# Kernel tuning notes

Hardware: AMD Instinct MI355X
Metric: run time of the kernel (lower is better)

## Reference

```python
import jax, jax.numpy as jnp
import numpy as np

N_NODES = 100000
N_EDGES = 600000
IN_CH = 128
HID = 64
NEG_SLOPE = 0.01  # nn.LeakyReLU default


def setup_inputs() -> dict:
    key = jax.random.key(0)
    k1, k2, k3, k4, k5, k6, k7, k8 = jax.random.split(key, 8)
    s1 = 1.0 / np.sqrt(IN_CH)
    s2 = 1.0 / np.sqrt(HID)
    return {
        "z": jax.random.normal(k1, (N_NODES, IN_CH), dtype=jnp.float32),
        "edge_index": jax.random.randint(k2, (2, N_EDGES), 0, N_NODES, dtype=jnp.int64),
        "W1l": jax.random.uniform(k3, (HID, IN_CH), jnp.float32, -s1, s1),
        "b1l": jax.random.uniform(k4, (HID,), jnp.float32, -s1, s1),
        "W1r": jax.random.uniform(k5, (HID, IN_CH), jnp.float32, -s1, s1),
        "b1r": jax.random.uniform(k6, (HID,), jnp.float32, -s1, s1),
        "W2": jax.random.uniform(k7, (1, HID), jnp.float32, -s2, s2),
        "b2": jax.random.uniform(k8, (1,), jnp.float32, -s2, s2),
    }


def reference(z, edge_index, W1l, b1l, W1r, b1r, W2, b2):
    # gather src/dst node features: [E, in_ch]
    zl = z[edge_index[0]]
    zr = z[edge_index[1]]
    # dual linear + add: [E, hid]
    h = jnp.einsum('ei,hi->eh', zl, W1l) + b1l + jnp.einsum('ei,hi->eh', zr, W1r) + b1r
    h = jnp.where(h >= 0, h, NEG_SLOPE * h)  # LeakyReLU
    out = jnp.einsum('eh,oh->eo', h, W2) + b2  # [E, 1]
    return jax.nn.sigmoid(out)
```

## Files before the change

### kernel.cpp

```cpp
#include <hip/hip_runtime.h>
#include <math.h>

#define N_NODES 100000
#define N_EDGES 600000
#define IN_CH 128
#define HID 64
#define NEG_SLOPE 0.01f

typedef float4 f4;
typedef unsigned short u16;
typedef unsigned int u32;
typedef __attribute__((ext_vector_type(8))) short bf16x8;
typedef __attribute__((ext_vector_type(4))) float f32x4;

__device__ __forceinline__ float lrelu(float x) {
    return fmaxf(x, NEG_SLOPE * x);
}
__device__ __forceinline__ float uasf(u32 w) { return __uint_as_float(w); }

__device__ __forceinline__ u32 cvt_pk(float lo, float hi) {
    u32 r;
    asm("v_cvt_pk_bf16_f32 %0, %1, %2" : "=v"(r) : "v"(lo), "v"(hi));
    return r;
}
__device__ __forceinline__ u16 f2bf(float f) {
    u32 x = __float_as_uint(f);
    return (u16)((x + 0x7fffu + ((x >> 16) & 1u)) >> 16);
}

__device__ __forceinline__ int load_idx(const void* ei, int is64, int pos) {
    if (is64) return (int)((const long long*)ei)[pos];
    return ((const int*)ei)[pos];
}

__global__ __launch_bounds__(256) void node_proj_kernel(
    const float* __restrict__ z, const float* __restrict__ W1l,
    const float* __restrict__ b1l, const float* __restrict__ W1r,
    const float* __restrict__ b1r, const u32* __restrict__ ei_words,
    int* __restrict__ flag, u16* __restrict__ pcomb) {
    __shared__ uint4 wt[128 * 16];
    __shared__ uint4 zt[64 * 16];
    __shared__ u32 red;

    const int tid = threadIdx.x;

    if (blockIdx.x == 0) {
        if (tid == 0) red = 0u;
        __syncthreads();
        u32 acc = 0u;
        #pragma unroll
        for (int i = 0; i < 8; ++i)
            acc |= ei_words[(i * 256 + tid) * 2 + 1];
        atomicOr(&red, acc);
        __syncthreads();
        if (tid == 0) *flag = (red == 0u) ? 1 : 0;
    }

    #pragma unroll
    for (int i = 0; i < 8; ++i) {
        int gidx = tid + i * 256;
        int row = gidx >> 4, gr = gidx & 15;
        const float* wsrc = (row < 64) ? (W1l + row * IN_CH)
                                       : (W1r + (row - 64) * IN_CH);
        f4 a = ((const f4*)wsrc)[gr * 2];
        f4 b = ((const f4*)wsrc)[gr * 2 + 1];
        uint4 p;
        p.x = cvt_pk(a.x, a.y); p.y = cvt_pk(a.z, a.w);
        p.z = cvt_pk(b.x, b.y); p.w = cvt_pk(b.z, b.w);
        wt[(row << 4) | (gr ^ (row & 15))] = p;
    }

    const int base = blockIdx.x * 64;
    #pragma unroll
    for (int i = 0; i < 4; ++i) {
        int gidx = tid + i * 256;
        int row = gidx >> 4, gr = gidx & 15;
        int node = base + row;
        if (node >= N_NODES) node = N_NODES - 1;
        f4 a = ((const f4*)z)[node * 32 + gr * 2];
        f4 b = ((const f4*)z)[node * 32 + gr * 2 + 1];
        uint4 p;
        p.x = cvt_pk(a.x, a.y); p.y = cvt_pk(a.z, a.w);
        p.z = cvt_pk(b.x, b.y); p.w = cvt_pk(b.z, b.w);
        zt[(row << 4) | (gr ^ (row & 15))] = p;
    }
    __syncthreads();

    const int wave = tid >> 6, lane = tid & 63;
    const int m = lane & 15, g = lane >> 4;

    f32x4 acc[4][2];
    #pragma unroll
    for (int n4 = 0; n4 < 4; ++n4)
        #pragma unroll
        for (int c2 = 0; c2 < 2; ++c2) acc[n4][c2] = {0.f, 0.f, 0.f, 0.f};

    #pragma unroll
    for (int kk = 0; kk < 4; ++kk) {
        const int gran = (kk << 2) | g;
        bf16x8 zf[4], wf[2];
        #pragma unroll
        for (int n4 = 0; n4 < 4; ++n4)
            zf[n4] = *(const bf16x8*)&zt[((((n4 << 4) | m)) << 4) | (gran ^ m)];
        #pragma unroll
        for (int c2 = 0; c2 < 2; ++c2) {
            int R = (wave << 5) + (c2 << 4) + m;
            wf[c2] = *(const bf16x8*)&wt[(R << 4) | (gran ^ m)];
        }
        #pragma unroll
        for (int n4 = 0; n4 < 4; ++n4)
            #pragma unroll
            for (int c2 = 0; c2 < 2; ++c2)
                acc[n4][c2] = __builtin_amdgcn_mfma_f32_16x16x32_bf16(
                    wf[c2], zf[n4], acc[n4][c2], 0, 0, 0);
    }

    const int colbase = wave << 5;
    #pragma unroll
    for (int c2 = 0; c2 < 2; ++c2) {
        const int col0 = colbase + (c2 << 4) + (g << 2);
        const float* bsrc = (colbase < 64) ? (b1l + col0) : (b1r + col0 - 64);
        f4 bb = *(const f4*)bsrc;
        #pragma unroll
        for (int n4 = 0; n4 < 4; ++n4) {
            int node = base + (n4 << 4) + m;
            if (node < N_NODES) {
                uint2 v;
                v.x = cvt_pk(acc[n4][c2][0] + bb.x, acc[n4][c2][1] + bb.y);
                v.y = cvt_pk(acc[n4][c2][2] + bb.z, acc[n4][c2][3] + bb.w);
                *(uint2*)(pcomb + (size_t)node * 128 + col0) = v;
            }
        }
    }
}

__device__ __forceinline__ float edot(uint4 a, uint4 b, f4 w0, f4 w1) {
    float s;
    s  = lrelu(uasf(a.x << 16) + uasf(b.x << 16)) * w0.x;
    s += lrelu(uasf(a.x & 0xffff0000u) + uasf(b.x & 0xffff0000u)) * w0.y;
    s += lrelu(uasf(a.y << 16) + uasf(b.y << 16)) * w0.z;
    s += lrelu(uasf(a.y & 0xffff0000u) + uasf(b.y & 0xffff0000u)) * w0.w;
    s += lrelu(uasf(a.z << 16) + uasf(b.z << 16)) * w1.x;
    s += lrelu(uasf(a.z & 0xffff0000u) + uasf(b.z & 0xffff0000u)) * w1.y;
    s += lrelu(uasf(a.w << 16) + uasf(b.w << 16)) * w1.z;
    s += lrelu(uasf(a.w & 0xffff0000u) + uasf(b.w & 0xffff0000u)) * w1.w;
    return s;
}

__global__ __launch_bounds__(256) void edge_kernel(
    const void* __restrict__ ei, const int* __restrict__ flag,
    const u16* __restrict__ pcomb, const float* __restrict__ W2,
    const float* __restrict__ b2, float* __restrict__ out) {
    int t = blockIdx.x * 256 + threadIdx.x;
    int pair = t >> 3;
    int c = t & 7;
    if (pair >= N_EDGES / 2) return;
    const int is64 = *flag;
    int s0, s1, d0, d1;
    if (is64) {
        const longlong2* p = (const longlong2*)ei;
        longlong2 sp = p[pair];
        longlong2 dp = p[N_EDGES / 2 + pair];
        s0 = (int)sp.x; s1 = (int)sp.y; d0 = (int)dp.x; d1 = (int)dp.y;
    } else {
        const int2* p = (const int2*)ei;
        int2 sp = p[pair];
        int2 dp = p[N_EDGES / 2 + pair];
        s0 = sp.x; s1 = sp.y; d0 = dp.x; d1 = dp.y;
    }
    const uint4* pc4 = (const uint4*)pcomb;
    uint4 a0 = pc4[s0 * 16 + c];
    uint4 b0 = pc4[d0 * 16 + 8 + c];
    uint4 a1 = pc4[s1 * 16 + c];
    uint4 b1 = pc4[d1 * 16 + 8 + c];
    f4 w0 = ((const f4*)W2)[c * 2];
    f4 w1 = ((const f4*)W2)[c * 2 + 1];
    float r0 = edot(a0, b0, w0, w1);
    float r1 = edot(a1, b1, w0, w1);
    r0 += __shfl_xor(r0, 4, 8);
    r0 += __shfl_xor(r0, 2, 8);
    r0 += __shfl_xor(r0, 1, 8);
    r1 += __shfl_xor(r1, 4, 8);
    r1 += __shfl_xor(r1, 2, 8);
    r1 += __shfl_xor(r1, 1, 8);
    if (c == 0) {
        float bb = b2[0];
        float2 o;
        o.x = 1.f / (1.f + __expf(-(r0 + bb)));
        o.y = 1.f / (1.f + __expf(-(r1 + bb)));
        *(float2*)(out + pair * 2) = o;
    }
}

__global__ void detect_idx_kernel(const u32* __restrict__ ei_words,
                                  int* __restrict__ flag) {
    __shared__ u32 red;
    if (threadIdx.x == 0) red = 0u;
    __syncthreads();
    u32 acc = 0u;
    #pragma unroll
    for (int i = 0; i < 8; ++i)
        acc |= ei_words[(i * 256 + threadIdx.x) * 2 + 1];
    atomicOr(&red, acc);
    __syncthreads();
    if (threadIdx.x == 0) *flag = (red == 0u) ? 1 : 0;
}

__global__ __launch_bounds__(256) void edge_fallback_kernel(
    const float* __restrict__ z, const void* __restrict__ ei,
    const int* __restrict__ flag, const float* __restrict__ W1l,
    const float* __restrict__ b1l, const float* __restrict__ W1r,
    const float* __restrict__ b1r, const float* __restrict__ W2,
    const float* __restrict__ b2, float* __restrict__ out) {
    __shared__ f4 Wl4[64 * 32];
    __shared__ f4 Wr4[64 * 32];
    const int tid = threadIdx.x;
    #pragma unroll
    for (int i = 0; i < 8; ++i) {
        int gg = tid + i * 256;
        int h = gg >> 5, v = gg & 31;
        int slot = (h << 5) | (v ^ (h & 7));
        Wl4[slot] = ((const f4*)W1l)[gg];
        Wr4[slot] = ((const f4*)W1r)[gg];
    }
    __syncthreads();
    const int wave = tid >> 6, lane = tid & 63;
    int e = blockIdx.x * 4 + wave;
    if (e >= N_EDGES) return;
    const int is64 = (flag != nullptr) ? *flag : 0;
    int src = load_idx(ei, is64, e);
    int dst = load_idx(ei, is64, N_EDGES + e);
    float accl = 0.f, accr = 0.f;
    #pragma unroll 4
    for (int v = 0; v < 32; ++v) {
        f4 wl = Wl4[(lane << 5) | (v ^ (lane & 7))];
        f4 wr = Wr4[(lane << 5) | (v ^ (lane & 7))];
        f4 zl = ((const f4*)z)[src * 32 + v];
        f4 zr = ((const f4*)z)[dst * 32 + v];
        accl += wl.x * zl.x + wl.y * zl.y + wl.z * zl.z + wl.w * zl.w;
        accr += wr.x * zr.x + wr.y * zr.y + wr.z * zr.z + wr.w * zr.w;
    }
    float h = lrelu(accl + b1l[lane] + accr + b1r[lane]) * W2[lane];
    #pragma unroll
    for (int off = 32; off; off >>= 1) h += __shfl_xor(h, off, 64);
    if (lane == 0) out[e] = 1.f / (1.f + __expf(-(h + b2[0])));
}

extern "C" void kernel_launch(void* const* d_in, const int* in_sizes, int n_in,
                              void* d_out, int out_size, void* d_ws,
                              size_t ws_size, hipStream_t stream) {
    const float* z   = (const float*)d_in[0];
    const void*  ei  = d_in[1];
    const float* W1l = (const float*)d_in[2];
    const float* b1l = (const float*)d_in[3];
    const float* W1r = (const float*)d_in[4];
    const float* b1r = (const float*)d_in[5];
    const float* W2  = (const float*)d_in[6];
    const float* b2  = (const float*)d_in[7];
    float* out = (float*)d_out;

    const size_t pcomb_bytes = (size_t)N_NODES * 128 * sizeof(u16);
    const size_t need = pcomb_bytes + 256;

    if (ws_size >= need) {
        u16* pcomb = (u16*)d_ws;
        int* flag = (int*)((char*)d_ws + pcomb_bytes);
        node_proj_kernel<<<(N_NODES + 63) / 64, 256, 0, stream>>>(
            z, W1l, b1l, W1r, b1r, (const u32*)ei, flag, pcomb);
        edge_kernel<<<(N_EDGES / 2 * 8 + 255) / 256, 256, 0, stream>>>(
            ei, flag, pcomb, W2, b2, out);
    } else if (ws_size >= 256) {
        int* flag = (int*)d_ws;
        detect_idx_kernel<<<1, 256, 0, stream>>>((const u32*)ei, flag);
        edge_fallback_kernel<<<(N_EDGES + 3) / 4, 256, 0, stream>>>(
            z, ei, flag, W1l, b1l, W1r, b1r, W2, b2, out);
    } else {
        edge_fallback_kernel<<<(N_EDGES + 3) / 4, 256, 0, stream>>>(
            z, ei, nullptr, W1l, b1l, W1r, b1r, W2, b2, out);
    }
}
```

Measured before the change: 45.67 us.

## Fuse node projection and edge scoring into one persistent cooperative kernel

Replaces the two-kernel path with a single cooperative persistent kernel. It loops over node tiles to compute the bf16 projections, waits at a grid-wide sync, then scores edges with a grid-stride loop handling four edges per 8-lane group. Each block detects the index width itself, so the weights are converted to bf16 in LDS once per block rather than once per tile, and one kernel launch is saved. The costs are a grid barrier, host-side occupancy queries on every call, and fewer resident blocks than the old launch for latency hiding. The fallback edge kernel also now processes four edges per group.

```diff
diff --git a/kernel.cpp b/kernel.cpp
--- a/kernel.cpp
+++ b/kernel.cpp
@@ -1,4 +1,5 @@
 #include <hip/hip_runtime.h>
+#include <hip/hip_cooperative_groups.h>
 #include <math.h>
 
 #define N_NODES 100000
@@ -23,37 +24,45 @@
     asm("v_cvt_pk_bf16_f32 %0, %1, %2" : "=v"(r) : "v"(lo), "v"(hi));
     return r;
 }
-__device__ __forceinline__ u16 f2bf(float f) {
-    u32 x = __float_as_uint(f);
-    return (u16)((x + 0x7fffu + ((x >> 16) & 1u)) >> 16);
-}
 
 __device__ __forceinline__ int load_idx(const void* ei, int is64, int pos) {
     if (is64) return (int)((const long long*)ei)[pos];
     return ((const int*)ei)[pos];
 }
 
-__global__ __launch_bounds__(256) void node_proj_kernel(
+__device__ __forceinline__ float edot(uint4 a, uint4 b, f4 w0, f4 w1) {
+    float s;
+    s  = lrelu(uasf(a.x << 16) + uasf(b.x << 16)) * w0.x;
+    s += lrelu(uasf(a.x & 0xffff0000u) + uasf(b.x & 0xffff0000u)) * w0.y;
+    s += lrelu(uasf(a.y << 16) + uasf(b.y << 16)) * w0.z;
+    s += lrelu(uasf(a.y & 0xffff0000u) + uasf(b.y & 0xffff0000u)) * w0.w;
+    s += lrelu(uasf(a.z << 16) + uasf(b.z << 16)) * w1.x;
+    s += lrelu(uasf(a.z & 0xffff0000u) + uasf(b.z & 0xffff0000u)) * w1.y;
+    s += lrelu(uasf(a.w << 16) + uasf(b.w << 16)) * w1.z;
+    s += lrelu(uasf(a.w & 0xffff0000u) + uasf(b.w & 0xffff0000u)) * w1.w;
+    return s;
+}
+
+__global__ __launch_bounds__(256) void fused_kernel(
     const float* __restrict__ z, const float* __restrict__ W1l,
     const float* __restrict__ b1l, const float* __restrict__ W1r,
-    const float* __restrict__ b1r, const u32* __restrict__ ei_words,
-    int* __restrict__ flag, u16* __restrict__ pcomb) {
+    const float* __restrict__ b1r, const void* __restrict__ ei,
+    const float* __restrict__ W2, const float* __restrict__ b2,
+    float* __restrict__ out, u16* __restrict__ pcomb) {
     __shared__ uint4 wt[128 * 16];
     __shared__ uint4 zt[64 * 16];
-    __shared__ u32 red;
+    __shared__ u32 sflag;
 
     const int tid = threadIdx.x;
 
-    if (blockIdx.x == 0) {
-        if (tid == 0) red = 0u;
-        __syncthreads();
+    if (tid == 0) sflag = 0u;
+    __syncthreads();
+    {
         u32 acc = 0u;
-        #pragma unroll
-        for (int i = 0; i < 8; ++i)
-            acc |= ei_words[(i * 256 + tid) * 2 + 1];
-        atomicOr(&red, acc);
-        __syncthreads();
-        if (tid == 0) *flag = (red == 0u) ? 1 : 0;
+        const u32* w = (const u32*)ei;
+        #pragma unroll
+        for (int i = 0; i < 8; ++i) acc |= w[(i * 256 + tid) * 2 + 1];
+        if (acc) atomicOr(&sflag, 1u);
     }
 
     #pragma unroll
@@ -70,6 +79,162 @@
         wt[(row << 4) | (gr ^ (row & 15))] = p;
     }
 
+    const int wave = tid >> 6, lane = tid & 63;
+    const int m = lane & 15, g = lane >> 4;
+
+    for (int tile = blockIdx.x; tile * 64 < N_NODES; tile += gridDim.x) {
+        const int base = tile * 64;
+        #pragma unroll
+        for (int i = 0; i < 4; ++i) {
+            int gidx = tid + i * 256;
+            int row = gidx >> 4, gr = gidx & 15;
+            int node = base + row;
+            if (node >= N_NODES) node = N_NODES - 1;
+            f4 a = ((const f4*)z)[node * 32 + gr * 2];
+            f4 b = ((const f4*)z)[node * 32 + gr * 2 + 1];
+            uint4 p;
+            p.x = cvt_pk(a.x, a.y); p.y = cvt_pk(a.z, a.w);
+            p.z = cvt_pk(b.x, b.y); p.w = cvt_pk(b.z, b.w);
+            zt[(row << 4) | (gr ^ (row & 15))] = p;
+        }
+        __syncthreads();
+
+        f32x4 acc[4][2];
+        #pragma unroll
+        for (int n4 = 0; n4 < 4; ++n4)
+            #pragma unroll
+            for (int c2 = 0; c2 < 2; ++c2) acc[n4][c2] = {0.f, 0.f, 0.f, 0.f};
+
+        #pragma unroll
+        for (int kk = 0; kk < 4; ++kk) {
+            const int gran = (kk << 2) | g;
+            bf16x8 zf[4], wf[2];
+            #pragma unroll
+            for (int n4 = 0; n4 < 4; ++n4)
+                zf[n4] = *(const bf16x8*)&zt[(((n4 << 4) | m) << 4) | (gran ^ m)];
+            #pragma unroll
+            for (int c2 = 0; c2 < 2; ++c2) {
+                int R = (wave << 5) + (c2 << 4) + m;
+                wf[c2] = *(const bf16x8*)&wt[(R << 4) | (gran ^ m)];
+            }
+            #pragma unroll
+            for (int n4 = 0; n4 < 4; ++n4)
+                #pragma unroll
+                for (int c2 = 0; c2 < 2; ++c2)
+                    acc[n4][c2] = __builtin_amdgcn_mfma_f32_16x16x32_bf16(
+                        wf[c2], zf[n4], acc[n4][c2], 0, 0, 0);
+        }
+
+        const int colbase = wave << 5;
+        #pragma unroll
+        for (int c2 = 0; c2 < 2; ++c2) {
+            const int col0 = colbase + (c2 << 4) + (g << 2);
+            const float* bsrc = (colbase < 64) ? (b1l + col0) : (b1r + col0 - 64);
+            f4 bb = *(const f4*)bsrc;
+            #pragma unroll
+            for (int n4 = 0; n4 < 4; ++n4) {
+                int node = base + (n4 << 4) + m;
+                if (node < N_NODES) {
+                    uint2 v;
+                    v.x = cvt_pk(acc[n4][c2][0] + bb.x, acc[n4][c2][1] + bb.y);
+                    v.y = cvt_pk(acc[n4][c2][2] + bb.z, acc[n4][c2][3] + bb.w);
+                    *(uint2*)(pcomb + (size_t)node * 128 + col0) = v;
+                }
+            }
+        }
+        __syncthreads();
+    }
+
+    const int is64 = (sflag == 0u);
+
+    cooperative_groups::this_grid().sync();
+
+    const int c = tid & 7;
+    const f4 w0 = ((const f4*)W2)[c * 2];
+    const f4 w1 = ((const f4*)W2)[c * 2 + 1];
+    const float bb = b2[0];
+    const int nthreads = gridDim.x * 256;
+    const int qstride = nthreads >> 3;
+    const int NQ = N_EDGES / 4;
+
+    for (int q = (blockIdx.x * 256 + tid) >> 3; q < NQ; q += qstride) {
+        int s[4], d[4];
+        if (is64) {
+            const longlong2* p = (const longlong2*)ei;
+            longlong2 p0 = p[2 * q], p1 = p[2 * q + 1];
+            longlong2 q0 = p[N_EDGES / 2 + 2 * q], q1 = p[N_EDGES / 2 + 2 * q + 1];
+            s[0] = (int)p0.x; s[1] = (int)p0.y; s[2] = (int)p1.x; s[3] = (int)p1.y;
+            d[0] = (int)q0.x; d[1] = (int)q0.y; d[2] = (int)q1.x; d[3] = (int)q1.y;
+        } else {
+            int4 sp = ((const int4*)ei)[q];
+            int4 dp = ((const int4*)ei)[N_EDGES / 4 + q];
+            s[0] = sp.x; s[1] = sp.y; s[2] = sp.z; s[3] = sp.w;
+            d[0] = dp.x; d[1] = dp.y; d[2] = dp.z; d[3] = dp.w;
+        }
+        const uint4* pc4 = (const uint4*)pcomb;
+        uint4 a0 = pc4[s[0] * 16 + c],     a1 = pc4[s[1] * 16 + c];
+        uint4 a2 = pc4[s[2] * 16 + c],     a3 = pc4[s[3] * 16 + c];
+        uint4 e0 = pc4[d[0] * 16 + 8 + c], e1 = pc4[d[1] * 16 + 8 + c];
+        uint4 e2 = pc4[d[2] * 16 + 8 + c], e3 = pc4[d[3] * 16 + 8 + c];
+        float r0 = edot(a0, e0, w0, w1);
+        float r1 = edot(a1, e1, w0, w1);
+        float r2 = edot(a2, e2, w0, w1);
+        float r3 = edot(a3, e3, w0, w1);
+        #pragma unroll
+        for (int off = 4; off; off >>= 1) {
+            r0 += __shfl_xor(r0, off, 8);
+            r1 += __shfl_xor(r1, off, 8);
+            r2 += __shfl_xor(r2, off, 8);
+            r3 += __shfl_xor(r3, off, 8);
+        }
+        if (c == 0) {
+            f4 o;
+            o.x = 1.f / (1.f + __expf(-(r0 + bb)));
+            o.y = 1.f / (1.f + __expf(-(r1 + bb)));
+            o.z = 1.f / (1.f + __expf(-(r2 + bb)));
+            o.w = 1.f / (1.f + __expf(-(r3 + bb)));
+            *(f4*)(out + q * 4) = o;
+        }
+    }
+}
+
+__global__ __launch_bounds__(256) void node_proj_kernel(
+    const float* __restrict__ z, const float* __restrict__ W1l,
+    const float* __restrict__ b1l, const float* __restrict__ W1r,
+    const float* __restrict__ b1r, const u32* __restrict__ ei_words,
+    int* __restrict__ flag, u16* __restrict__ pcomb) {
+    __shared__ uint4 wt[128 * 16];
+    __shared__ uint4 zt[64 * 16];
+    __shared__ u32 red;
+
+    const int tid = threadIdx.x;
+
+    if (blockIdx.x == 0) {
+        if (tid == 0) red = 0u;
+        __syncthreads();
+        u32 acc = 0u;
+        #pragma unroll
+        for (int i = 0; i < 8; ++i)
+            acc |= ei_words[(i * 256 + tid) * 2 + 1];
+        atomicOr(&red, acc);
+        __syncthreads();
+        if (tid == 0) *flag = (red == 0u) ? 1 : 0;
+    }
+
+    #pragma unroll
+    for (int i = 0; i < 8; ++i) {
+        int gidx = tid + i * 256;
+        int row = gidx >> 4, gr = gidx & 15;
+        const float* wsrc = (row < 64) ? (W1l + row * IN_CH)
+                                       : (W1r + (row - 64) * IN_CH);
+        f4 a = ((const f4*)wsrc)[gr * 2];
+        f4 b = ((const f4*)wsrc)[gr * 2 + 1];
+        uint4 p;
+        p.x = cvt_pk(a.x, a.y); p.y = cvt_pk(a.z, a.w);
+        p.z = cvt_pk(b.x, b.y); p.w = cvt_pk(b.z, b.w);
+        wt[(row << 4) | (gr ^ (row & 15))] = p;
+    }
+
     const int base = blockIdx.x * 64;
     #pragma unroll
     for (int i = 0; i < 4; ++i) {
@@ -101,7 +266,7 @@
         bf16x8 zf[4], wf[2];
         #pragma unroll
         for (int n4 = 0; n4 < 4; ++n4)
-            zf[n4] = *(const bf16x8*)&zt[((((n4 << 4) | m)) << 4) | (gran ^ m)];
+            zf[n4] = *(const bf16x8*)&zt[(((n4 << 4) | m) << 4) | (gran ^ m)];
         #pragma unroll
         for (int c2 = 0; c2 < 2; ++c2) {
             int R = (wave << 5) + (c2 << 4) + m;
@@ -134,61 +299,54 @@
     }
 }
 
-__device__ __forceinline__ float edot(uint4 a, uint4 b, f4 w0, f4 w1) {
-    float s;
-    s  = lrelu(uasf(a.x << 16) + uasf(b.x << 16)) * w0.x;
-    s += lrelu(uasf(a.x & 0xffff0000u) + uasf(b.x & 0xffff0000u)) * w0.y;
-    s += lrelu(uasf(a.y << 16) + uasf(b.y << 16)) * w0.z;
-    s += lrelu(uasf(a.y & 0xffff0000u) + uasf(b.y & 0xffff0000u)) * w0.w;
-    s += lrelu(uasf(a.z << 16) + uasf(b.z << 16)) * w1.x;
-    s += lrelu(uasf(a.z & 0xffff0000u) + uasf(b.z & 0xffff0000u)) * w1.y;
-    s += lrelu(uasf(a.w << 16) + uasf(b.w << 16)) * w1.z;
-    s += lrelu(uasf(a.w & 0xffff0000u) + uasf(b.w & 0xffff0000u)) * w1.w;
-    return s;
-}
-
-__global__ __launch_bounds__(256) void edge_kernel(
+__global__ __launch_bounds__(256) void edge_quad_kernel(
     const void* __restrict__ ei, const int* __restrict__ flag,
     const u16* __restrict__ pcomb, const float* __restrict__ W2,
     const float* __restrict__ b2, float* __restrict__ out) {
     int t = blockIdx.x * 256 + threadIdx.x;
-    int pair = t >> 3;
+    int q = t >> 3;
     int c = t & 7;
-    if (pair >= N_EDGES / 2) return;
+    if (q >= N_EDGES / 4) return;
     const int is64 = *flag;
-    int s0, s1, d0, d1;
+    int s[4], d[4];
     if (is64) {
         const longlong2* p = (const longlong2*)ei;
-        longlong2 sp = p[pair];
-        longlong2 dp = p[N_EDGES / 2 + pair];
-        s0 = (int)sp.x; s1 = (int)sp.y; d0 = (int)dp.x; d1 = (int)dp.y;
+        longlong2 p0 = p[2 * q], p1 = p[2 * q + 1];
+        longlong2 q0 = p[N_EDGES / 2 + 2 * q], q1 = p[N_EDGES / 2 + 2 * q + 1];
+        s[0] = (int)p0.x; s[1] = (int)p0.y; s[2] = (int)p1.x; s[3] = (int)p1.y;
+        d[0] = (int)q0.x; d[1] = (int)q0.y; d[2] = (int)q1.x; d[3] = (int)q1.y;
     } else {
-        const int2* p = (const int2*)ei;
-        int2 sp = p[pair];
-        int2 dp = p[N_EDGES / 2 + pair];
-        s0 = sp.x; s1 = sp.y; d0 = dp.x; d1 = dp.y;
+        int4 sp = ((const int4*)ei)[q];
+        int4 dp = ((const int4*)ei)[N_EDGES / 4 + q];
+        s[0] = sp.x; s[1] = sp.y; s[2] = sp.z; s[3] = sp.w;
+        d[0] = dp.x; d[1] = dp.y; d[2] = dp.z; d[3] = dp.w;
     }
     const uint4* pc4 = (const uint4*)pcomb;
-    uint4 a0 = pc4[s0 * 16 + c];
-    uint4 b0 = pc4[d0 * 16 + 8 + c];
-    uint4 a1 = pc4[s1 * 16 + c];
-    uint4 b1 = pc4[d1 * 16 + 8 + c];
+    uint4 a0 = pc4[s[0] * 16 + c],     a1 = pc4[s[1] * 16 + c];
+    uint4 a2 = pc4[s[2] * 16 + c],     a3 = pc4[s[3] * 16 + c];
+    uint4 e0 = pc4[d[0] * 16 + 8 + c], e1 = pc4[d[1] * 16 + 8 + c];
+    uint4 e2 = pc4[d[2] * 16 + 8 + c], e3 = pc4[d[3] * 16 + 8 + c];
     f4 w0 = ((const f4*)W2)[c * 2];
     f4 w1 = ((const f4*)W2)[c * 2 + 1];
-    float r0 = edot(a0, b0, w0, w1);
-    float r1 = edot(a1, b1, w0, w1);
-    r0 += __shfl_xor(r0, 4, 8);
-    r0 += __shfl_xor(r0, 2, 8);
-    r0 += __shfl_xor(r0, 1, 8);
-    r1 += __shfl_xor(r1, 4, 8);
-    r1 += __shfl_xor(r1, 2, 8);
-    r1 += __shfl_xor(r1, 1, 8);
+    float r0 = edot(a0, e0, w0, w1);
+    float r1 = edot(a1, e1, w0, w1);
+    float r2 = edot(a2, e2, w0, w1);
+    float r3 = edot(a3, e3, w0, w1);
+    #pragma unroll
+    for (int off = 4; off; off >>= 1) {
+        r0 += __shfl_xor(r0, off, 8);
+        r1 += __shfl_xor(r1, off, 8);
+        r2 += __shfl_xor(r2, off, 8);
+        r3 += __shfl_xor(r3, off, 8);
+    }
     if (c == 0) {
         float bb = b2[0];
-        float2 o;
+        f4 o;
         o.x = 1.f / (1.f + __expf(-(r0 + bb)));
         o.y = 1.f / (1.f + __expf(-(r1 + bb)));
-        *(float2*)(out + pair * 2) = o;
+        o.z = 1.f / (1.f + __expf(-(r2 + bb)));
+        o.w = 1.f / (1.f + __expf(-(r3 + bb)));
+        *(f4*)(out + q * 4) = o;
     }
 }
 
@@ -265,10 +423,27 @@
     if (ws_size >= need) {
         u16* pcomb = (u16*)d_ws;
         int* flag = (int*)((char*)d_ws + pcomb_bytes);
-        node_proj_kernel<<<(N_NODES + 63) / 64, 256, 0, stream>>>(
-            z, W1l, b1l, W1r, b1r, (const u32*)ei, flag, pcomb);
-        edge_kernel<<<(N_EDGES / 2 * 8 + 255) / 256, 256, 0, stream>>>(
-            ei, flag, pcomb, W2, b2, out);
+
+        int maxB = 0, nCU = 0, dev = 0;
+        hipGetDevice(&dev);
+        hipDeviceGetAttribute(&nCU, hipDeviceAttributeMultiprocessorCount, dev);
+        hipOccupancyMaxActiveBlocksPerMultiprocessor(&maxB, fused_kernel, 256, 0);
+        int grid = (maxB > 0 && nCU > 0) ? maxB * nCU : 0;
+
+        hipError_t e = hipErrorUnknown;
+        if (grid >= 64) {
+            void* args[] = {(void*)&z,  (void*)&W1l, (void*)&b1l, (void*)&W1r,
+                            (void*)&b1r, (void*)&ei, (void*)&W2,  (void*)&b2,
+                            (void*)&out, (void*)&pcomb};
+            e = hipLaunchCooperativeKernel((const void*)fused_kernel, dim3(grid),
+                                           dim3(256), args, 0, stream);
+        }
+        if (e != hipSuccess) {
+            node_proj_kernel<<<(N_NODES + 63) / 64, 256, 0, stream>>>(
+                z, W1l, b1l, W1r, b1r, (const u32*)ei, flag, pcomb);
+            edge_quad_kernel<<<(N_EDGES / 4 * 8 + 255) / 256, 256, 0, stream>>>(
+                ei, flag, pcomb, W2, b2, out);
+        }
     } else if (ws_size >= 256) {
         int* flag = (int*)d_ws;
         detect_idx_kernel<<<1, 256, 0, stream>>>((const u32*)ei, flag);
```

New measurement: 105.3 us. +130.6%, slower.

## Persistent node projection with register-resident weights; process four edges per thread group

Applied to the files above, without the earlier changes.

The node projection becomes a persistent grid of 1024 blocks that converts W1l/W1r to bf16 once into registers and then loops over node tiles. Before, every one of ~1563 blocks reloaded and converted the full weight matrix through LDS. The edge kernel now handles four edges per 8-lane group instead of two, using wider index loads and float4 output stores to get more memory-level parallelism. The cost is more registers per thread, which can lower occupancy, and fewer blocks in the edge kernel.

```diff
diff --git a/kernel.cpp b/kernel.cpp
--- a/kernel.cpp
+++ b/kernel.cpp
@@ -6,6 +6,7 @@
 #define IN_CH 128
 #define HID 64
 #define NEG_SLOPE 0.01f
+#define NP_GRID 1024
 
 typedef float4 f4;
 typedef unsigned short u16;
@@ -23,115 +24,10 @@
     asm("v_cvt_pk_bf16_f32 %0, %1, %2" : "=v"(r) : "v"(lo), "v"(hi));
     return r;
 }
-__device__ __forceinline__ u16 f2bf(float f) {
-    u32 x = __float_as_uint(f);
-    return (u16)((x + 0x7fffu + ((x >> 16) & 1u)) >> 16);
-}
 
 __device__ __forceinline__ int load_idx(const void* ei, int is64, int pos) {
     if (is64) return (int)((const long long*)ei)[pos];
     return ((const int*)ei)[pos];
-}
-
-__global__ __launch_bounds__(256) void node_proj_kernel(
-    const float* __restrict__ z, const float* __restrict__ W1l,
-    const float* __restrict__ b1l, const float* __restrict__ W1r,
-    const float* __restrict__ b1r, const u32* __restrict__ ei_words,
-    int* __restrict__ flag, u16* __restrict__ pcomb) {
-    __shared__ uint4 wt[128 * 16];
-    __shared__ uint4 zt[64 * 16];
-    __shared__ u32 red;
-
-    const int tid = threadIdx.x;
-
-    if (blockIdx.x == 0) {
-        if (tid == 0) red = 0u;
-        __syncthreads();
-        u32 acc = 0u;
-        #pragma unroll
-        for (int i = 0; i < 8; ++i)
-            acc |= ei_words[(i * 256 + tid) * 2 + 1];
-        atomicOr(&red, acc);
-        __syncthreads();
-        if (tid == 0) *flag = (red == 0u) ? 1 : 0;
-    }
-
-    #pragma unroll
-    for (int i = 0; i < 8; ++i) {
-        int gidx = tid + i * 256;
-        int row = gidx >> 4, gr = gidx & 15;
-        const float* wsrc = (row < 64) ? (W1l + row * IN_CH)
-                                       : (W1r + (row - 64) * IN_CH);
-        f4 a = ((const f4*)wsrc)[gr * 2];
-        f4 b = ((const f4*)wsrc)[gr * 2 + 1];
-        uint4 p;
-        p.x = cvt_pk(a.x, a.y); p.y = cvt_pk(a.z, a.w);
-        p.z = cvt_pk(b.x, b.y); p.w = cvt_pk(b.z, b.w);
-        wt[(row << 4) | (gr ^ (row & 15))] = p;
-    }
-
-    const int base = blockIdx.x * 64;
-    #pragma unroll
-    for (int i = 0; i < 4; ++i) {
-        int gidx = tid + i * 256;
-        int row = gidx >> 4, gr = gidx & 15;
-        int node = base + row;
-        if (node >= N_NODES) node = N_NODES - 1;
-        f4 a = ((const f4*)z)[node * 32 + gr * 2];
-        f4 b = ((const f4*)z)[node * 32 + gr * 2 + 1];
-        uint4 p;
-        p.x = cvt_pk(a.x, a.y); p.y = cvt_pk(a.z, a.w);
-        p.z = cvt_pk(b.x, b.y); p.w = cvt_pk(b.z, b.w);
-        zt[(row << 4) | (gr ^ (row & 15))] = p;
-    }
-    __syncthreads();
-
-    const int wave = tid >> 6, lane = tid & 63;
-    const int m = lane & 15, g = lane >> 4;
-
-    f32x4 acc[4][2];
-    #pragma unroll
-    for (int n4 = 0; n4 < 4; ++n4)
-        #pragma unroll
-        for (int c2 = 0; c2 < 2; ++c2) acc[n4][c2] = {0.f, 0.f, 0.f, 0.f};
-
-    #pragma unroll
-    for (int kk = 0; kk < 4; ++kk) {
-        const int gran = (kk << 2) | g;
-        bf16x8 zf[4], wf[2];
-        #pragma unroll
-        for (int n4 = 0; n4 < 4; ++n4)
-            zf[n4] = *(const bf16x8*)&zt[((((n4 << 4) | m)) << 4) | (gran ^ m)];
-        #pragma unroll
-        for (int c2 = 0; c2 < 2; ++c2) {
-            int R = (wave << 5) + (c2 << 4) + m;
-            wf[c2] = *(const bf16x8*)&wt[(R << 4) | (gran ^ m)];
-        }
-        #pragma unroll
-        for (int n4 = 0; n4 < 4; ++n4)
-            #pragma unroll
-            for (int c2 = 0; c2 < 2; ++c2)
-                acc[n4][c2] = __builtin_amdgcn_mfma_f32_16x16x32_bf16(
-                    wf[c2], zf[n4], acc[n4][c2], 0, 0, 0);
-    }
-
-    const int colbase = wave << 5;
-    #pragma unroll
-    for (int c2 = 0; c2 < 2; ++c2) {
-        const int col0 = colbase + (c2 << 4) + (g << 2);
-        const float* bsrc = (colbase < 64) ? (b1l + col0) : (b1r + col0 - 64);
-        f4 bb = *(const f4*)bsrc;
-        #pragma unroll
-        for (int n4 = 0; n4 < 4; ++n4) {
-            int node = base + (n4 << 4) + m;
-            if (node < N_NODES) {
-                uint2 v;
-                v.x = cvt_pk(acc[n4][c2][0] + bb.x, acc[n4][c2][1] + bb.y);
-                v.y = cvt_pk(acc[n4][c2][2] + bb.z, acc[n4][c2][3] + bb.w);
-                *(uint2*)(pcomb + (size_t)node * 128 + col0) = v;
-            }
-        }
-    }
 }
 
 __device__ __forceinline__ float edot(uint4 a, uint4 b, f4 w0, f4 w1) {
@@ -147,48 +43,164 @@
     return s;
 }
 
-__global__ __launch_bounds__(256) void edge_kernel(
+__global__ __launch_bounds__(256) void node_proj_v2(
+    const float* __restrict__ z, const float* __restrict__ W1l,
+    const float* __restrict__ b1l, const float* __restrict__ W1r,
+    const float* __restrict__ b1r, const u32* __restrict__ ei_words,
+    int* __restrict__ flag, u16* __restrict__ pcomb) {
+    __shared__ uint4 zt[64 * 16];
+    __shared__ u32 red;
+
+    const int tid = threadIdx.x;
+
+    if (blockIdx.x == 0) {
+        if (tid == 0) red = 0u;
+        __syncthreads();
+        u32 acc = 0u;
+        #pragma unroll
+        for (int i = 0; i < 8; ++i)
+            acc |= ei_words[(i * 256 + tid) * 2 + 1];
+        atomicOr(&red, acc);
+        __syncthreads();
+        if (tid == 0) *flag = (red == 0u) ? 1 : 0;
+    }
+
+    const int wave = tid >> 6, lane = tid & 63;
+    const int m = lane & 15, g = lane >> 4;
+
+    bf16x8 wf[2][4];
+    #pragma unroll
+    for (int c2 = 0; c2 < 2; ++c2) {
+        const int R = (wave << 5) + (c2 << 4) + m;
+        const float* wsrc = (R < 64) ? (W1l + R * IN_CH)
+                                     : (W1r + (R - 64) * IN_CH);
+        #pragma unroll
+        for (int kk = 0; kk < 4; ++kk) {
+            const int gran = (kk << 2) | g;
+            f4 a = ((const f4*)wsrc)[gran * 2];
+            f4 b = ((const f4*)wsrc)[gran * 2 + 1];
+            uint4 p;
+            p.x = cvt_pk(a.x, a.y); p.y = cvt_pk(a.z, a.w);
+            p.z = cvt_pk(b.x, b.y); p.w = cvt_pk(b.z, b.w);
+            wf[c2][kk] = *(const bf16x8*)&p;
+        }
+    }
+
+    const int colbase = wave << 5;
+    f4 bb[2];
+    #pragma unroll
+    for (int c2 = 0; c2 < 2; ++c2) {
+        const int col0 = colbase + (c2 << 4) + (g << 2);
+        bb[c2] = *(const f4*)((colbase < 64) ? (b1l + col0) : (b1r + col0 - 64));
+    }
+
+    const int ntiles = (N_NODES + 63) / 64;
+    for (int tile = blockIdx.x; tile < ntiles; tile += NP_GRID) {
+        const int base = tile * 64;
+        __syncthreads();
+        #pragma unroll
+        for (int i = 0; i < 4; ++i) {
+            int gidx = tid + i * 256;
+            int row = gidx >> 4, gr = gidx & 15;
+            int node = base + row;
+            if (node >= N_NODES) node = N_NODES - 1;
+            f4 a = ((const f4*)z)[node * 32 + gr * 2];
+            f4 b = ((const f4*)z)[node * 32 + gr * 2 + 1];
+            uint4 p;
+            p.x = cvt_pk(a.x, a.y); p.y = cvt_pk(a.z, a.w);
+            p.z = cvt_pk(b.x, b.y); p.w = cvt_pk(b.z, b.w);
+            zt[(row << 4) | (gr ^ (row & 15))] = p;
+        }
+        __syncthreads();
+
+        f32x4 acc[4][2];
+        #pragma unroll
+        for (int n4 = 0; n4 < 4; ++n4)
+            #pragma unroll
+            for (int c2 = 0; c2 < 2; ++c2) acc[n4][c2] = {0.f, 0.f, 0.f, 0.f};
+
+        #pragma unroll
+        for (int kk = 0; kk < 4; ++kk) {
+            const int gran = (kk << 2) | g;
+            bf16x8 zf[4];
+            #pragma unroll
+            for (int n4 = 0; n4 < 4; ++n4)
+                zf[n4] = *(const bf16x8*)&zt[(((n4 << 4) | m) << 4) | (gran ^ m)];
+            #pragma unroll
+            for (int n4 = 0; n4 < 4; ++n4)
+                #pragma unroll
+                for (int c2 = 0; c2 < 2; ++c2)
+                    acc[n4][c2] = __builtin_amdgcn_mfma_f32_16x16x32_bf16(
+                        wf[c2][kk], zf[n4], acc[n4][c2], 0, 0, 0);
+        }
+
+        #pragma unroll
+        for (int c2 = 0; c2 < 2; ++c2) {
+            const int col0 = colbase + (c2 << 4) + (g << 2);
+            #pragma unroll
+            for (int n4 = 0; n4 < 4; ++n4) {
+                int node = base + (n4 << 4) + m;
+                if (node < N_NODES) {
+                    uint2 v;
+                    v.x = cvt_pk(acc[n4][c2][0] + bb[c2].x,
+                                 acc[n4][c2][1] + bb[c2].y);
+                    v.y = cvt_pk(acc[n4][c2][2] + bb[c2].z,
+                                 acc[n4][c2][3] + bb[c2].w);
+                    *(uint2*)(pcomb + (size_t)node * 128 + col0) = v;
+                }
+            }
+        }
+    }
+}
+
+__global__ __launch_bounds__(256) void edge_quad_kernel(
     const void* __restrict__ ei, const int* __restrict__ flag,
     const u16* __restrict__ pcomb, const float* __restrict__ W2,
     const float* __restrict__ b2, float* __restrict__ out) {
     int t = blockIdx.x * 256 + threadIdx.x;
-    int pair = t >> 3;
+    int q = t >> 3;
     int c = t & 7;
-    if (pair >= N_EDGES / 2) return;
+    if (q >= N_EDGES / 4) return;
     const int is64 = *flag;
-    int s0, s1, d0, d1;
+    int s[4], d[4];
     if (is64) {
         const longlong2* p = (const longlong2*)ei;
-        longlong2 sp = p[pair];
-        longlong2 dp = p[N_EDGES / 2 + pair];
-        s0 = (int)sp.x; s1 = (int)sp.y; d0 = (int)dp.x; d1 = (int)dp.y;
+        longlong2 p0 = p[2 * q], p1 = p[2 * q + 1];
+        longlong2 q0 = p[N_EDGES / 2 + 2 * q], q1 = p[N_EDGES / 2 + 2 * q + 1];
+        s[0] = (int)p0.x; s[1] = (int)p0.y; s[2] = (int)p1.x; s[3] = (int)p1.y;
+        d[0] = (int)q0.x; d[1] = (int)q0.y; d[2] = (int)q1.x; d[3] = (int)q1.y;
     } else {
-        const int2* p = (const int2*)ei;
-        int2 sp = p[pair];
-        int2 dp = p[N_EDGES / 2 + pair];
-        s0 = sp.x; s1 = sp.y; d0 = dp.x; d1 = dp.y;
+        int4 sp = ((const int4*)ei)[q];
+        int4 dp = ((const int4*)ei)[N_EDGES / 4 + q];
+        s[0] = sp.x; s[1] = sp.y; s[2] = sp.z; s[3] = sp.w;
+        d[0] = dp.x; d[1] = dp.y; d[2] = dp.z; d[3] = dp.w;
     }
     const uint4* pc4 = (const uint4*)pcomb;
-    uint4 a0 = pc4[s0 * 16 + c];
-    uint4 b0 = pc4[d0 * 16 + 8 + c];
-    uint4 a1 = pc4[s1 * 16 + c];
-    uint4 b1 = pc4[d1 * 16 + 8 + c];
+    uint4 a0 = pc4[s[0] * 16 + c],     a1 = pc4[s[1] * 16 + c];
+    uint4 a2 = pc4[s[2] * 16 + c],     a3 = pc4[s[3] * 16 + c];
+    uint4 e0 = pc4[d[0] * 16 + 8 + c], e1 = pc4[d[1] * 16 + 8 + c];
+    uint4 e2 = pc4[d[2] * 16 + 8 + c], e3 = pc4[d[3] * 16 + 8 + c];
     f4 w0 = ((const f4*)W2)[c * 2];
     f4 w1 = ((const f4*)W2)[c * 2 + 1];
-    float r0 = edot(a0, b0, w0, w1);
-    float r1 = edot(a1, b1, w0, w1);
-    r0 += __shfl_xor(r0, 4, 8);
-    r0 += __shfl_xor(r0, 2, 8);
-    r0 += __shfl_xor(r0, 1, 8);
-    r1 += __shfl_xor(r1, 4, 8);
-    r1 += __shfl_xor(r1, 2, 8);
-    r1 += __shfl_xor(r1, 1, 8);
+    float r0 = edot(a0, e0, w0, w1);
+    float r1 = edot(a1, e1, w0, w1);
+    float r2 = edot(a2, e2, w0, w1);
+    float r3 = edot(a3, e3, w0, w1);
+    #pragma unroll
+    for (int off = 4; off; off >>= 1) {
+        r0 += __shfl_xor(r0, off, 8);
+        r1 += __shfl_xor(r1, off, 8);
+        r2 += __shfl_xor(r2, off, 8);
+        r3 += __shfl_xor(r3, off, 8);
+    }
     if (c == 0) {
-        float bb = b2[0];
-        float2 o;
-        o.x = 1.f / (1.f + __expf(-(r0 + bb)));
-        o.y = 1.f / (1.f + __expf(-(r1 + bb)));
-        *(float2*)(out + pair * 2) = o;
+        float bbs = b2[0];
+        f4 o;
+        o.x = 1.f / (1.f + __expf(-(r0 + bbs)));
+        o.y = 1.f / (1.f + __expf(-(r1 + bbs)));
+        o.z = 1.f / (1.f + __expf(-(r2 + bbs)));
+        o.w = 1.f / (1.f + __expf(-(r3 + bbs)));
+        *(f4*)(out + q * 4) = o;
     }
 }
 
@@ -265,9 +277,9 @@
     if (ws_size >= need) {
         u16* pcomb = (u16*)d_ws;
         int* flag = (int*)((char*)d_ws + pcomb_bytes);
-        node_proj_kernel<<<(N_NODES + 63) / 64, 256, 0, stream>>>(
+        node_proj_v2<<<NP_GRID, 256, 0, stream>>>(
             z, W1l, b1l, W1r, b1r, (const u32*)ei, flag, pcomb);
-        edge_kernel<<<(N_EDGES / 2 * 8 + 255) / 256, 256, 0, stream>>>(
+        edge_quad_kernel<<<(N_EDGES / 4 * 8 + 255) / 256, 256, 0, stream>>>(
             ei, flag, pcomb, W2, b2, out);
     } else if (ws_size >= 256) {
         int* flag = (int*)d_ws;
```

Result: slower. 47.29 us (+3.5%).
